# Performance work log

Measured on AMD Instinct MI355X. Metric: run time of the kernel, lower is better.

Reference implementation:

```python
import jax, jax.numpy as jnp
import numpy as np

N_FACET = 8
EMB_DIM = 64
N_ITER = 3
EPS = 1e-12

def _l2norm(v, axis):
    n = jnp.sqrt(jnp.sum(v * v, axis=axis, keepdims=True))
    return v / jnp.maximum(n, EPS)

def setup_inputs() -> dict:
    key = jax.random.key(0)
    k1, k2 = jax.random.split(key)
    B, NB = 2048, 64
    features = jax.random.normal(k1, (B, N_FACET * EMB_DIM), dtype=jnp.float32)
    metapath_features = jax.random.normal(k2, (B, NB, N_FACET * EMB_DIM), dtype=jnp.float32)
    return {"features": features, "metapath_features": metapath_features}

def reference(features, metapath_features):
    B = features.shape[0]
    NB = metapath_features.shape[1]
    x = features.reshape(B, N_FACET, EMB_DIM)            # [B,F,D]
    z = metapath_features.reshape(B, NB, N_FACET, EMB_DIM)  # [B,N,F,D]
    x = _l2norm(x, axis=2)
    z = _l2norm(z, axis=3)
    u = x
    for it in range(N_ITER):
        # p[b,n,f] = sum_d z[b,n,f,d] * u[b,f,d]
        p = jnp.einsum('bnfd,bfd->bnf', z, u)
        p = jax.nn.softmax(p, axis=2)
        # u[b,f,d] = sum_n z[b,n,f,d] * p[b,n,f]
        u = jnp.einsum('bnfd,bnf->bfd', z, p) + x
        if it < N_ITER - 1:
            u = _l2norm(u, axis=2)
    return u.reshape(B, N_FACET * EMB_DIM)
```

## Files before the change

### kernel.cpp

```cpp
#include <hip/hip_runtime.h>

typedef unsigned int u32;

using half2v = decltype(__builtin_amdgcn_cvt_pkrtz(0.f, 0.f));

__device__ inline u32 h2u(half2v h) { return __builtin_bit_cast(u32, h); }
__device__ inline half2v u2h(u32 u) { return __builtin_bit_cast(half2v, u); }

template <int CTRL>
__device__ inline float dppf(float x) {
  return __builtin_bit_cast(
      float, __builtin_amdgcn_update_dpp(0, __builtin_bit_cast(int, x), CTRL,
                                         0xF, 0xF, true));
}

__device__ inline float rlane(float v, int l) {
  return __builtin_bit_cast(
      float, __builtin_amdgcn_readlane(__builtin_bit_cast(int, v), l));
}

#if __has_builtin(__builtin_amdgcn_fdot2)
__device__ inline float fdot2f(half2v a, half2v b, float c) {
  return __builtin_amdgcn_fdot2(a, b, c, false);
}
#else
__device__ inline float fdot2f(half2v a, half2v b, float c) {
  return c + (float)a.x * (float)b.x + (float)a.y * (float)b.y;
}
#endif

__device__ inline float row16_sum(float v) {
  v += dppf<0x121>(v);
  v += dppf<0x122>(v);
  v += dppf<0x124>(v);
  v += dppf<0x128>(v);
  return v;
}

__device__ inline float max8(float v) {
  v = fmaxf(v, dppf<0xB1>(v));
  v = fmaxf(v, dppf<0x4E>(v));
  v = fmaxf(v, dppf<0x141>(v));
  return v;
}
__device__ inline float sum8(float v) {
  v += dppf<0xB1>(v);
  v += dppf<0x4E>(v);
  v += dppf<0x141>(v);
  return v;
}

__global__ __launch_bounds__(512, 4) void hete_attn(
    const float* __restrict__ feat, const float* __restrict__ mp,
    float* __restrict__ outp) {
  __shared__ u32 z_lds[512 * 32];
  __shared__ u32 u_lds[8 * 36];
  __shared__ float p_lds[64 * 9 + 4];

  const int t = threadIdx.x;
  const int b = blockIdx.x;

  float2 xreg = make_float2(0.f, 0.f);
  if (t < 256) {
    const float2* xg = (const float2*)(feat + (size_t)b * 512);
    float2 xv = xg[t];
    float ss = row16_sum(xv.x * xv.x + xv.y * xv.y);
    ss += __shfl_xor(ss, 16);
    float sc = 1.0f / fmaxf(sqrtf(ss), 1e-12f);
    xreg.x = xv.x * sc;
    xreg.y = xv.y * sc;
    int f = t >> 5, d2 = t & 31;
    u_lds[f * 36 + d2] = h2u(__builtin_amdgcn_cvt_pkrtz(xreg.x, xreg.y));
  }

  {
    const float4* zg = (const float4*)(mp + (size_t)b * 32768);
    for (int hv = 0; hv < 2; hv++) {
      float4 v[8];
#pragma unroll
      for (int j = 0; j < 8; j++) v[j] = zg[(hv * 8 + j) * 512 + t];
#pragma unroll
      for (int j = 0; j < 8; j++) {
        int i = hv * 8 + j;
        float4 q = v[j];
        float ss = row16_sum(q.x * q.x + q.y * q.y + q.z * q.z + q.w * q.w);
        float sc = 1.0f / fmaxf(sqrtf(ss), 1e-12f);
        half2v h0 = __builtin_amdgcn_cvt_pkrtz(q.x * sc, q.y * sc);
        half2v h1 = __builtin_amdgcn_cvt_pkrtz(q.z * sc, q.w * sc);
        int row = i * 32 + (t >> 4);
        int c4 = t & 15;
        int dw = row * 32 + ((((c4 >> 1) ^ (row & 7)) << 2) + ((c4 & 1) << 1));
        uint2 pk;
        pk.x = h2u(h0);
        pk.y = h2u(h1);
        *(uint2*)&z_lds[dw] = pk;
      }
    }
  }
  __syncthreads();

  const int fq = t & 7;
  const int nq = t >> 3;
  const int uf = t >> 5;
  const int d2 = t & 31;
  const int lane = t & 63;

  for (int it = 0; it < 3; it++) {
    {
      float acc = 0.f;
      const u32* zrow = &z_lds[t * 32];
      const u32* urow = &u_lds[fq * 36];
#pragma unroll
      for (int c = 0; c < 8; c++) {
        uint4 zq = *(const uint4*)(zrow + ((c ^ fq) << 2));
        uint4 uq = *(const uint4*)(urow + (c << 2));
        acc = fdot2f(u2h(zq.x), u2h(uq.x), acc);
        acc = fdot2f(u2h(zq.y), u2h(uq.y), acc);
        acc = fdot2f(u2h(zq.z), u2h(uq.z), acc);
        acc = fdot2f(u2h(zq.w), u2h(uq.w), acc);
      }
      float m = max8(acc);
      float e = __expf(acc - m);
      float s = sum8(e);
      p_lds[nq * 9 + fq] = e / s;
    }
    __syncthreads();

    if (t < 256) {
      float pA = p_lds[lane * 9 + (uf & 6)];
      float pB = p_lds[lane * 9 + (uf | 1)];
      float2 acc2 = xreg;
      const u32* zc = &z_lds[uf * 32 + ((((d2 >> 2) ^ uf) << 2) + (d2 & 3))];
      const bool lo = lane < 32;
#pragma unroll 8
      for (int n = 0; n < 64; n++) {
        half2v hz = u2h(zc[n << 8]);
        float pf = lo ? rlane(pA, n) : rlane(pB, n);
        acc2.x += (float)hz.x * pf;
        acc2.y += (float)hz.y * pf;
      }
      if (it < 2) {
        float ss = row16_sum(acc2.x * acc2.x + acc2.y * acc2.y);
        ss += __shfl_xor(ss, 16);
        float sc = 1.0f / fmaxf(sqrtf(ss), 1e-12f);
        u_lds[uf * 36 + d2] =
            h2u(__builtin_amdgcn_cvt_pkrtz(acc2.x * sc, acc2.y * sc));
      } else {
        *(float2*)&outp[((size_t)b << 9) + (uf << 6) + (d2 << 1)] = acc2;
      }
    }
    __syncthreads();
  }
}

extern "C" void kernel_launch(void* const* d_in, const int* in_sizes, int n_in,
                              void* d_out, int out_size, void* d_ws,
                              size_t ws_size, hipStream_t stream) {
  const float* feat = (const float*)d_in[0];
  const float* mp = (const float*)d_in[1];
  float* outp = (float*)d_out;
  int B = in_sizes[0] / 512;
  hete_attn<<<B, 512, 0, stream>>>(feat, mp, outp);
}
```

Before: 397.9 us.

## Split the u-update reduction over all 512 threads and cache z rows in registers

The second einsum (u = z^T p) now uses all 512 threads instead of 256. Each thread handles an 8-neighbour slice times 8 dims with vectorized 128-bit LDS reads, then reduces across the 8-thread group with DPP. The serial 64-step loop of readlane broadcasts goes away, and p is stored transposed so it can be read as float4. Each thread's z row for the p-score dot product is held in 32 registers across iterations rather than reread from LDS, and x moves to LDS. The costs are higher register pressure under the 512x4 launch bounds and extra cross-lane reduction work.

```diff
diff --git a/kernel.cpp b/kernel.cpp
--- a/kernel.cpp
+++ b/kernel.cpp
@@ -12,11 +12,6 @@
   return __builtin_bit_cast(
       float, __builtin_amdgcn_update_dpp(0, __builtin_bit_cast(int, x), CTRL,
                                          0xF, 0xF, true));
-}
-
-__device__ inline float rlane(float v, int l) {
-  return __builtin_bit_cast(
-      float, __builtin_amdgcn_readlane(__builtin_bit_cast(int, v), l));
 }
 
 #if __has_builtin(__builtin_amdgcn_fdot2)
@@ -55,22 +50,22 @@
     float* __restrict__ outp) {
   __shared__ u32 z_lds[512 * 32];
   __shared__ u32 u_lds[8 * 36];
-  __shared__ float p_lds[64 * 9 + 4];
+  __shared__ float p_lds[8 * 72];
+  __shared__ float x_lds[512];
 
   const int t = threadIdx.x;
   const int b = blockIdx.x;
 
-  float2 xreg = make_float2(0.f, 0.f);
   if (t < 256) {
     const float2* xg = (const float2*)(feat + (size_t)b * 512);
     float2 xv = xg[t];
     float ss = row16_sum(xv.x * xv.x + xv.y * xv.y);
     ss += __shfl_xor(ss, 16);
     float sc = 1.0f / fmaxf(sqrtf(ss), 1e-12f);
-    xreg.x = xv.x * sc;
-    xreg.y = xv.y * sc;
-    int f = t >> 5, d2 = t & 31;
-    u_lds[f * 36 + d2] = h2u(__builtin_amdgcn_cvt_pkrtz(xreg.x, xreg.y));
+    float x0 = xv.x * sc, x1 = xv.y * sc;
+    x_lds[2 * t] = x0;
+    x_lds[2 * t + 1] = x1;
+    u_lds[(t >> 5) * 36 + (t & 31)] = h2u(__builtin_amdgcn_cvt_pkrtz(x0, x1));
   }
 
   {
@@ -101,52 +96,92 @@
 
   const int fq = t & 7;
   const int nq = t >> 3;
-  const int uf = t >> 5;
-  const int d2 = t & 31;
-  const int lane = t & 63;
+
+  const int uf = t >> 6;
+  const int uc = (t >> 3) & 7;
+  const int ug = t & 7;
+
+  uint4 zrow[8];
+  {
+    const u32* zrowp = &z_lds[t * 32];
+#pragma unroll
+    for (int c = 0; c < 8; c++)
+      zrow[c] = *(const uint4*)(zrowp + ((c ^ fq) << 2));
+  }
+
+  const u32* zcolp = &z_lds[ug * 2048 + uf * 32 + ((uc ^ uf) << 2)];
+  const float* pcolp = &p_lds[uf * 72 + ug * 8];
+  const float* xp = &x_lds[uf * 64 + uc * 8];
 
   for (int it = 0; it < 3; it++) {
     {
+      const u32* urow = &u_lds[fq * 36];
       float acc = 0.f;
-      const u32* zrow = &z_lds[t * 32];
-      const u32* urow = &u_lds[fq * 36];
 #pragma unroll
       for (int c = 0; c < 8; c++) {
-        uint4 zq = *(const uint4*)(zrow + ((c ^ fq) << 2));
         uint4 uq = *(const uint4*)(urow + (c << 2));
-        acc = fdot2f(u2h(zq.x), u2h(uq.x), acc);
-        acc = fdot2f(u2h(zq.y), u2h(uq.y), acc);
-        acc = fdot2f(u2h(zq.z), u2h(uq.z), acc);
-        acc = fdot2f(u2h(zq.w), u2h(uq.w), acc);
+        acc = fdot2f(u2h(zrow[c].x), u2h(uq.x), acc);
+        acc = fdot2f(u2h(zrow[c].y), u2h(uq.y), acc);
+        acc = fdot2f(u2h(zrow[c].z), u2h(uq.z), acc);
+        acc = fdot2f(u2h(zrow[c].w), u2h(uq.w), acc);
       }
       float m = max8(acc);
       float e = __expf(acc - m);
       float s = sum8(e);
-      p_lds[nq * 9 + fq] = e / s;
+      p_lds[fq * 72 + nq] = e / s;
     }
     __syncthreads();
 
-    if (t < 256) {
-      float pA = p_lds[lane * 9 + (uf & 6)];
-      float pB = p_lds[lane * 9 + (uf | 1)];
-      float2 acc2 = xreg;
-      const u32* zc = &z_lds[uf * 32 + ((((d2 >> 2) ^ uf) << 2) + (d2 & 3))];
-      const bool lo = lane < 32;
-#pragma unroll 8
-      for (int n = 0; n < 64; n++) {
-        half2v hz = u2h(zc[n << 8]);
-        float pf = lo ? rlane(pA, n) : rlane(pB, n);
-        acc2.x += (float)hz.x * pf;
-        acc2.y += (float)hz.y * pf;
+    {
+      float pk[8];
+      *(float4*)&pk[0] = *(const float4*)(pcolp);
+      *(float4*)&pk[4] = *(const float4*)(pcolp + 4);
+      float acc[8] = {0.f, 0.f, 0.f, 0.f, 0.f, 0.f, 0.f, 0.f};
+#pragma unroll
+      for (int k = 0; k < 8; k++) {
+        uint4 zq = *(const uint4*)(zcolp + (k << 8));
+        half2v h0 = u2h(zq.x), h1 = u2h(zq.y), h2 = u2h(zq.z), h3 = u2h(zq.w);
+        float p = pk[k];
+        acc[0] += (float)h0.x * p;
+        acc[1] += (float)h0.y * p;
+        acc[2] += (float)h1.x * p;
+        acc[3] += (float)h1.y * p;
+        acc[4] += (float)h2.x * p;
+        acc[5] += (float)h2.y * p;
+        acc[6] += (float)h3.x * p;
+        acc[7] += (float)h3.y * p;
       }
+#pragma unroll
+      for (int j = 0; j < 8; j++) acc[j] = sum8(acc[j]);
+      float4 xa = *(const float4*)(xp);
+      float4 xb = *(const float4*)(xp + 4);
+      acc[0] += xa.x; acc[1] += xa.y; acc[2] += xa.z; acc[3] += xa.w;
+      acc[4] += xb.x; acc[5] += xb.y; acc[6] += xb.z; acc[7] += xb.w;
+
       if (it < 2) {
-        float ss = row16_sum(acc2.x * acc2.x + acc2.y * acc2.y);
+        float ss = 0.f;
+#pragma unroll
+        for (int j = 0; j < 8; j++) ss += acc[j] * acc[j];
+        ss = row16_sum(ss);
         ss += __shfl_xor(ss, 16);
-        float sc = 1.0f / fmaxf(sqrtf(ss), 1e-12f);
-        u_lds[uf * 36 + d2] =
-            h2u(__builtin_amdgcn_cvt_pkrtz(acc2.x * sc, acc2.y * sc));
+        ss += __shfl_xor(ss, 32);
+        float sc = 1.0f / fmaxf(sqrtf(ss * 0.125f), 1e-12f);
+        if (ug == 0) {
+          uint4 o;
+          o.x = h2u(__builtin_amdgcn_cvt_pkrtz(acc[0] * sc, acc[1] * sc));
+          o.y = h2u(__builtin_amdgcn_cvt_pkrtz(acc[2] * sc, acc[3] * sc));
+          o.z = h2u(__builtin_amdgcn_cvt_pkrtz(acc[4] * sc, acc[5] * sc));
+          o.w = h2u(__builtin_amdgcn_cvt_pkrtz(acc[6] * sc, acc[7] * sc));
+          *(uint4*)&u_lds[uf * 36 + (uc << 2)] = o;
+        }
       } else {
-        *(float2*)&outp[((size_t)b << 9) + (uf << 6) + (d2 << 1)] = acc2;
+        if (ug == 0) {
+          float* op = &outp[((size_t)b << 9) + (uf << 6) + (uc << 3)];
+          float4 o1 = {acc[0], acc[1], acc[2], acc[3]};
+          float4 o2 = {acc[4], acc[5], acc[6], acc[7]};
+          *(float4*)op = o1;
+          *(float4*)(op + 4) = o2;
+        }
       }
     }
     __syncthreads();
```

After: 365.6 us. 1.09x faster.
